# Performance work log

Hardware: AMD Instinct MI355X
Metric: run time of the kernel (lower is better)

Reference implementation:

```python
import jax, jax.numpy as jnp
import numpy as np

RATE = 0.5
N_NODES = 4096
N_EDGES = 131072
D_FEAT = 512


def setup_inputs() -> dict:
    key = jax.random.key(0)
    k1, k2, k3 = jax.random.split(key, 3)
    x = jax.random.normal(k1, (N_NODES, D_FEAT), dtype=jnp.float32)
    edge_index = jax.random.randint(k2, (2, N_EDGES), 0, N_NODES, dtype=jnp.int32)
    attention = jax.random.normal(k3, (N_EDGES, 1), dtype=jnp.float32)
    batch = jnp.zeros((N_NODES,), dtype=jnp.int32)
    return {"x": x, "edge_index": edge_index, "attention": attention,
            "batch": batch, "direction": 1}


def reference(x, edge_index, attention, batch, direction):
    N = x.shape[0]
    src = edge_index[0]
    dst = edge_index[1]

    # degree = torch.bincount(e_batch) over source nodes
    degree = jax.ops.segment_sum(jnp.ones_like(src, dtype=jnp.float32), src,
                                 num_segments=N)
    # g_pooling = segment mean of per-edge attention grouped by source node
    att_sum = jax.ops.segment_sum(attention[:, 0], src, num_segments=N)
    att_mean = jnp.where(degree > 0, att_sum / jnp.maximum(degree, 1.0), 0.0)
    # node_scores = direction * mean_attention * degree
    node_scores = direction * att_mean * degree

    # topk with ratio (single graph => k = ceil(rate * N)), sorted descending
    k = int(np.ceil(RATE * N))
    _, perm = jax.lax.top_k(node_scores, k)  # [k]

    # augment_adj: spspmm(A, A) -> 2-hop path counts; weights None -> ones
    A = jnp.zeros((N, N), dtype=jnp.float32).at[src, dst].add(1.0)
    A2 = A @ A  # [N, N] path counts; edges of augmented graph = nonzeros

    # filter_adj: keep edges among selected nodes, reindexed to [0, k)
    adj = (A2[perm][:, perm] > 0).astype(jnp.float32)  # [k, k] dense edge mask

    x_pooled = x[perm]            # [k, D]
    batch_pooled = batch[perm]    # [k]
    return (x_pooled, adj, batch_pooled, perm.reshape(1, -1))
```

## Files before the change

### kernel.cpp

```cpp
#include <hip/hip_runtime.h>

#define N_NODES 4096
#define N_EDGES 131072
#define D_FEAT  512
#define K_SEL   2048
#define MAXDEG  128
#define NWORDS  128

__global__ void zero_cnt(unsigned* __restrict__ cnt) {
    cnt[blockIdx.x * 256 + threadIdx.x] = 0u;
}

__global__ void build_kernel(const int* __restrict__ src, const int* __restrict__ dst,
                             unsigned* __restrict__ cnt, unsigned* __restrict__ slots) {
    int e = blockIdx.x * 512 + threadIdx.x;
    int s = src[e];
    int d = dst[e];
    unsigned pos = atomicAdd(&cnt[s], 1u);
    if (pos < MAXDEG) slots[((unsigned)s << 7) + pos] = ((unsigned)e << 12) | (unsigned)d;
}

__global__ void score_kernel(const unsigned* __restrict__ cnt,
                             const unsigned* __restrict__ slots,
                             const float* __restrict__ att,
                             const int* __restrict__ dir_p,
                             float* __restrict__ scores,
                             unsigned* __restrict__ B) {
    __shared__ float a_ord[4][MAXDEG];
    __shared__ unsigned brow[4][NWORDS];
    int t = threadIdx.x, wave = t >> 6, lane = t & 63;
    int n = blockIdx.x * 4 + wave;
    unsigned nb = (unsigned)n << 7;
    unsigned d = min(cnt[n], (unsigned)MAXDEG);
    unsigned v0 = (lane < (int)d)        ? slots[nb + lane]      : 0xFFFFFFFFu;
    unsigned v1 = ((lane + 64) < (int)d) ? slots[nb + lane + 64] : 0xFFFFFFFFu;

    brow[wave][lane] = 0u;
    brow[wave][lane + 64] = 0u;
    if (lane < (int)d)        atomicOr(&brow[wave][(v0 & 0xFFFu) >> 5], 1u << (v0 & 31));
    if ((lane + 64) < (int)d) atomicOr(&brow[wave][(v1 & 0xFFFu) >> 5], 1u << (v1 & 31));

    int r0 = 0, r1 = 0;
    int dk = (d < 64u) ? (int)d : 64;
    if (d <= 64u) {
        for (int k = 0; k < dk; ++k) {
            unsigned a = __shfl(v0, k);
            r0 += (a < v0);
        }
    } else {
        for (int k = 0; k < dk; ++k) {
            unsigned a = __shfl(v0, k);
            unsigned b = __shfl(v1, k);
            r0 += (a < v0) + (b < v0);
            r1 += (a < v1) + (b < v1);
        }
    }
    if (lane < (int)d)        a_ord[wave][r0] = att[v0 >> 12];
    if ((lane + 64) < (int)d) a_ord[wave][r1] = att[v1 >> 12];
    __syncthreads();

    B[nb + lane] = brow[wave][lane];
    B[nb + lane + 64] = brow[wave][lane + 64];

    if (lane == 0) {
        float sum = 0.0f;
        for (unsigned i = 0; i < d; ++i) sum += a_ord[wave][i];
        float score = 0.0f;
        if (d > 0) {
            float df = (float)d;
            float mean = sum / df;
            score = ((float)dir_p[0] * mean) * df;
        }
        scores[n] = score;
    }
}

__global__ void rank_kernel(const float* __restrict__ scores,
                            const int* __restrict__ batch,
                            const float* __restrict__ x,
                            unsigned* __restrict__ permw,
                            float* __restrict__ out_x,
                            float* __restrict__ out_batch,
                            float* __restrict__ out_perm) {
    int t = threadIdx.x, wave = t >> 6, lane = t & 63;
    int n = blockIdx.x * 4 + wave;
    float s = scores[n];
    const float4* sc4 = (const float4*)scores;
    int r = 0;
    #pragma unroll
    for (int i = 0; i < 16; ++i) {
        int q = lane + (i << 6);
        float4 v = sc4[q];
        int m = q << 2;
        r += (v.x > s) || (v.x == s && (m + 0) < n);
        r += (v.y > s) || (v.y == s && (m + 1) < n);
        r += (v.z > s) || (v.z == s && (m + 2) < n);
        r += (v.w > s) || (v.w == s && (m + 3) < n);
    }
    #pragma unroll
    for (int off = 32; off; off >>= 1) r += __shfl_down(r, off);
    r = __shfl(r, 0);
    if (r < K_SEL) {
        if (lane == 0) {
            permw[r] = (unsigned)n;
            out_perm[r] = (float)n;
            out_batch[r] = (float)batch[n];
        }
        const float4* xs = (const float4*)(x + (size_t)n * D_FEAT);
        float4* od = (float4*)(out_x + (size_t)r * D_FEAT);
        od[lane] = xs[lane];
        od[lane + 64] = xs[lane + 64];
    }
}

__global__ void adj_kernel(const unsigned* __restrict__ permw,
                           const unsigned* __restrict__ cnt,
                           const unsigned* __restrict__ slots,
                           const unsigned* __restrict__ B,
                           float* __restrict__ out_adj) {
    __shared__ unsigned nbr[MAXDEG];
    __shared__ unsigned rowH[2][NWORDS];
    int p = blockIdx.x, t = threadIdx.x;
    unsigned n = permw[p];
    unsigned d = min(cnt[n], (unsigned)MAXDEG);
    if (t < (int)d) nbr[t] = slots[((size_t)n << 7) + t] & 0xFFFu;
    __syncthreads();
    int w = t & 127, h = t >> 7;
    unsigned acc = 0;
    for (unsigned i = (unsigned)h; i < d; i += 2)
        acc |= B[((size_t)nbr[i] << 7) + w];
    rowH[h][w] = acc;
    __syncthreads();
    if (t < NWORDS) rowH[0][t] |= rowH[1][t];
    __syncthreads();
    float4* o4 = (float4*)(out_adj + (size_t)p * K_SEL);
    #pragma unroll
    for (int i = 0; i < 2; ++i) {
        int q4 = t + (i << 8);
        int q = q4 << 2;
        unsigned c0 = permw[q], c1 = permw[q + 1], c2 = permw[q + 2], c3 = permw[q + 3];
        float4 v;
        v.x = (float)((rowH[0][c0 >> 5] >> (c0 & 31)) & 1u);
        v.y = (float)((rowH[0][c1 >> 5] >> (c1 & 31)) & 1u);
        v.z = (float)((rowH[0][c2 >> 5] >> (c2 & 31)) & 1u);
        v.w = (float)((rowH[0][c3 >> 5] >> (c3 & 31)) & 1u);
        o4[q4] = v;
    }
}

extern "C" void kernel_launch(void* const* d_in, const int* in_sizes, int n_in,
                              void* d_out, int out_size, void* d_ws, size_t ws_size,
                              hipStream_t stream) {
    const float* x     = (const float*)d_in[0];
    const int*   eidx  = (const int*)d_in[1];
    const float* att   = (const float*)d_in[2];
    const int*   batch = (const int*)d_in[3];
    const int*   dir_p = (const int*)d_in[4];
    const int* src = eidx;
    const int* dst = eidx + N_EDGES;

    char* ws = (char*)d_ws;
    unsigned* B      = (unsigned*)(ws + 0);
    unsigned* cnt    = (unsigned*)(ws + 2097152);
    float*    scores = (float*)   (ws + 2113536);
    unsigned* permw  = (unsigned*)(ws + 2129920);
    unsigned* slots  = (unsigned*)(ws + 2138112);

    float* out_x     = (float*)d_out;
    float* out_adj   = out_x + (size_t)K_SEL * D_FEAT;
    float* out_batch = out_adj + (size_t)K_SEL * K_SEL;
    float* out_perm  = out_batch + K_SEL;

    zero_cnt<<<N_NODES / 256, 256, 0, stream>>>(cnt);
    build_kernel<<<N_EDGES / 512, 512, 0, stream>>>(src, dst, cnt, slots);
    score_kernel<<<N_NODES / 4, 256, 0, stream>>>(cnt, slots, att, dir_p, scores, B);
    rank_kernel<<<N_NODES / 4, 256, 0, stream>>>(scores, batch, x, permw,
                                                 out_x, out_batch, out_perm);
    adj_kernel<<<K_SEL, 256, 0, stream>>>(permw, cnt, slots, B, out_adj);
}
```

Baseline: 43.57 us.

## Fuse count, build and score into one node-owning kernel with shared-memory bucketing

Replaces the zero, global-atomic bucket build and score kernels with one kernel where each block owns 32 source nodes. The block scans the full src array and buckets matching edges into shared memory with shared atomics, then computes scores and bitmask rows. This removes two launches and the global atomics and slot round-trip, but every block now rereads the whole edge list and only 128 blocks are launched.

New measurement: 121.5 us. +178.8%, slower.

```diff
diff --git a/kernel.cpp b/kernel.cpp
--- a/kernel.cpp
+++ b/kernel.cpp
@@ -6,72 +6,97 @@
 #define K_SEL   2048
 #define MAXDEG  128
 #define NWORDS  128
-
-__global__ void zero_cnt(unsigned* __restrict__ cnt) {
-    cnt[blockIdx.x * 256 + threadIdx.x] = 0u;
-}
-
-__global__ void build_kernel(const int* __restrict__ src, const int* __restrict__ dst,
-                             unsigned* __restrict__ cnt, unsigned* __restrict__ slots) {
-    int e = blockIdx.x * 512 + threadIdx.x;
-    int s = src[e];
-    int d = dst[e];
-    unsigned pos = atomicAdd(&cnt[s], 1u);
-    if (pos < MAXDEG) slots[((unsigned)s << 7) + pos] = ((unsigned)e << 12) | (unsigned)d;
-}
-
-__global__ void score_kernel(const unsigned* __restrict__ cnt,
-                             const unsigned* __restrict__ slots,
-                             const float* __restrict__ att,
-                             const int* __restrict__ dir_p,
-                             float* __restrict__ scores,
-                             unsigned* __restrict__ B) {
-    __shared__ float a_ord[4][MAXDEG];
+#define OWN     32
+#define NBSS    (N_NODES / OWN)
+
+__global__ __launch_bounds__(256) void bss_kernel(
+    const int* __restrict__ src, const int* __restrict__ dst,
+    const float* __restrict__ att, const int* __restrict__ dir_p,
+    unsigned* __restrict__ cnt, unsigned* __restrict__ gslots,
+    unsigned* __restrict__ B, float* __restrict__ scores)
+{
+    __shared__ unsigned lcnt[OWN];
+    __shared__ unsigned lslots[OWN][MAXDEG];
+    __shared__ float    a_ord[4][MAXDEG];
     __shared__ unsigned brow[4][NWORDS];
-    int t = threadIdx.x, wave = t >> 6, lane = t & 63;
-    int n = blockIdx.x * 4 + wave;
-    unsigned nb = (unsigned)n << 7;
-    unsigned d = min(cnt[n], (unsigned)MAXDEG);
-    unsigned v0 = (lane < (int)d)        ? slots[nb + lane]      : 0xFFFFFFFFu;
-    unsigned v1 = ((lane + 64) < (int)d) ? slots[nb + lane + 64] : 0xFFFFFFFFu;
-
-    brow[wave][lane] = 0u;
-    brow[wave][lane + 64] = 0u;
-    if (lane < (int)d)        atomicOr(&brow[wave][(v0 & 0xFFFu) >> 5], 1u << (v0 & 31));
-    if ((lane + 64) < (int)d) atomicOr(&brow[wave][(v1 & 0xFFFu) >> 5], 1u << (v1 & 31));
-
-    int r0 = 0, r1 = 0;
-    int dk = (d < 64u) ? (int)d : 64;
-    if (d <= 64u) {
-        for (int k = 0; k < dk; ++k) {
-            unsigned a = __shfl(v0, k);
-            r0 += (a < v0);
+    const int t = threadIdx.x, wave = t >> 6, lane = t & 63;
+    const int base = blockIdx.x * OWN;
+
+    if (t < OWN) lcnt[t] = 0u;
+    __syncthreads();
+
+    const int4* s4 = (const int4*)src;
+    for (int i = t; i < N_EDGES / 4; i += 256) {
+        int4 v = s4[i];
+        int e0 = i << 2;
+        unsigned ls;
+        ls = (unsigned)(v.x - base);
+        if (ls < OWN) { unsigned p = atomicAdd(&lcnt[ls], 1u);
+            if (p < MAXDEG) lslots[ls][p] = ((unsigned)(e0 + 0) << 12) | (unsigned)dst[e0 + 0]; }
+        ls = (unsigned)(v.y - base);
+        if (ls < OWN) { unsigned p = atomicAdd(&lcnt[ls], 1u);
+            if (p < MAXDEG) lslots[ls][p] = ((unsigned)(e0 + 1) << 12) | (unsigned)dst[e0 + 1]; }
+        ls = (unsigned)(v.z - base);
+        if (ls < OWN) { unsigned p = atomicAdd(&lcnt[ls], 1u);
+            if (p < MAXDEG) lslots[ls][p] = ((unsigned)(e0 + 2) << 12) | (unsigned)dst[e0 + 2]; }
+        ls = (unsigned)(v.w - base);
+        if (ls < OWN) { unsigned p = atomicAdd(&lcnt[ls], 1u);
+            if (p < MAXDEG) lslots[ls][p] = ((unsigned)(e0 + 3) << 12) | (unsigned)dst[e0 + 3]; }
+    }
+    __syncthreads();
+
+    for (int it = 0; it < OWN / 4; ++it) {
+        __syncthreads();
+        int ln = (it << 2) + wave;
+        int n = base + ln;
+        unsigned d = min(lcnt[ln], (unsigned)MAXDEG);
+        unsigned v0 = (lane < (int)d)        ? lslots[ln][lane]      : 0xFFFFFFFFu;
+        unsigned v1 = ((lane + 64) < (int)d) ? lslots[ln][lane + 64] : 0xFFFFFFFFu;
+
+        float a0 = (lane < (int)d)        ? att[v0 >> 12] : 0.0f;
+        float a1 = ((lane + 64) < (int)d) ? att[v1 >> 12] : 0.0f;
+
+        brow[wave][lane] = 0u;
+        brow[wave][lane + 64] = 0u;
+        if (lane < (int)d)        atomicOr(&brow[wave][(v0 & 0xFFFu) >> 5], 1u << (v0 & 31));
+        if ((lane + 64) < (int)d) atomicOr(&brow[wave][(v1 & 0xFFFu) >> 5], 1u << (v1 & 31));
+
+        int r0 = 0, r1 = 0;
+        int dk = (d < 64u) ? (int)d : 64;
+        if (d <= 64u) {
+            for (int k = 0; k < dk; ++k) {
+                unsigned a = __shfl(v0, k);
+                r0 += (a < v0);
+            }
+        } else {
+            for (int k = 0; k < dk; ++k) {
+                unsigned a = __shfl(v0, k);
+                unsigned b = __shfl(v1, k);
+                r0 += (a < v0) + (b < v0);
+                r1 += (a < v1) + (b < v1);
+            }
         }
-    } else {
-        for (int k = 0; k < dk; ++k) {
-            unsigned a = __shfl(v0, k);
-            unsigned b = __shfl(v1, k);
-            r0 += (a < v0) + (b < v0);
-            r1 += (a < v1) + (b < v1);
+        if (lane < (int)d)        a_ord[wave][r0] = a0;
+        if ((lane + 64) < (int)d) a_ord[wave][r1] = a1;
+        __syncthreads();
+
+        if (lane == 0) {
+            float sum = 0.0f;
+            for (unsigned i = 0; i < d; ++i) sum += a_ord[wave][i];
+            float score = 0.0f;
+            if (d > 0) {
+                float df = (float)d;
+                float mean = sum / df;
+                score = ((float)dir_p[0] * mean) * df;
+            }
+            scores[n] = score;
+            cnt[n] = d;
         }
-    }
-    if (lane < (int)d)        a_ord[wave][r0] = att[v0 >> 12];
-    if ((lane + 64) < (int)d) a_ord[wave][r1] = att[v1 >> 12];
-    __syncthreads();
-
-    B[nb + lane] = brow[wave][lane];
-    B[nb + lane + 64] = brow[wave][lane + 64];
-
-    if (lane == 0) {
-        float sum = 0.0f;
-        for (unsigned i = 0; i < d; ++i) sum += a_ord[wave][i];
-        float score = 0.0f;
-        if (d > 0) {
-            float df = (float)d;
-            float mean = sum / df;
-            score = ((float)dir_p[0] * mean) * df;
-        }
-        scores[n] = score;
+        unsigned nb = (unsigned)n << 7;
+        B[nb + lane] = brow[wave][lane];
+        B[nb + lane + 64] = brow[wave][lane + 64];
+        if (lane < (int)d)        gslots[nb + lane] = v0;
+        if ((lane + 64) < (int)d) gslots[nb + lane + 64] = v1;
     }
 }
 
@@ -164,17 +189,15 @@
     unsigned* cnt    = (unsigned*)(ws + 2097152);
     float*    scores = (float*)   (ws + 2113536);
     unsigned* permw  = (unsigned*)(ws + 2129920);
-    unsigned* slots  = (unsigned*)(ws + 2138112);
+    unsigned* gslots = (unsigned*)(ws + 2138112);
 
     float* out_x     = (float*)d_out;
     float* out_adj   = out_x + (size_t)K_SEL * D_FEAT;
     float* out_batch = out_adj + (size_t)K_SEL * K_SEL;
     float* out_perm  = out_batch + K_SEL;
 
-    zero_cnt<<<N_NODES / 256, 256, 0, stream>>>(cnt);
-    build_kernel<<<N_EDGES / 512, 512, 0, stream>>>(src, dst, cnt, slots);
-    score_kernel<<<N_NODES / 4, 256, 0, stream>>>(cnt, slots, att, dir_p, scores, B);
+    bss_kernel<<<NBSS, 256, 0, stream>>>(src, dst, att, dir_p, cnt, gslots, B, scores);
     rank_kernel<<<N_NODES / 4, 256, 0, stream>>>(scores, batch, x, permw,
                                                  out_x, out_batch, out_perm);
-    adj_kernel<<<K_SEL, 256, 0, stream>>>(permw, cnt, slots, B, out_adj);
-}
+    adj_kernel<<<K_SEL, 256, 0, stream>>>(permw, cnt, gslots, B, out_adj);
+}
```

## Drop precomputed neighbor bitmask; build 2-hop rows from slots with LDS atomics

Applied to the files above, without the earlier changes.

Removes the per-node adjacency bitmask array B (2 MB) that score_kernel wrote and adj_kernel read. adj_kernel now gathers each neighbor's destination list directly from slots and sets bits in one shared row with LDS atomicOr, instead of OR-ing 128-word bitmask rows. The aim is to cut global write and read traffic for B. The cost is more scattered slot reads, an extra cnt lookup per neighbor, and LDS atomic contention. score_kernel also issues the attention gathers earlier and sums in float4 chunks.

Result: slower. 46.08 us (+5.8%).

```diff
diff --git a/kernel.cpp b/kernel.cpp
--- a/kernel.cpp
+++ b/kernel.cpp
@@ -24,10 +24,8 @@
                              const unsigned* __restrict__ slots,
                              const float* __restrict__ att,
                              const int* __restrict__ dir_p,
-                             float* __restrict__ scores,
-                             unsigned* __restrict__ B) {
+                             float* __restrict__ scores) {
     __shared__ float a_ord[4][MAXDEG];
-    __shared__ unsigned brow[4][NWORDS];
     int t = threadIdx.x, wave = t >> 6, lane = t & 63;
     int n = blockIdx.x * 4 + wave;
     unsigned nb = (unsigned)n << 7;
@@ -35,10 +33,8 @@
     unsigned v0 = (lane < (int)d)        ? slots[nb + lane]      : 0xFFFFFFFFu;
     unsigned v1 = ((lane + 64) < (int)d) ? slots[nb + lane + 64] : 0xFFFFFFFFu;
 
-    brow[wave][lane] = 0u;
-    brow[wave][lane + 64] = 0u;
-    if (lane < (int)d)        atomicOr(&brow[wave][(v0 & 0xFFFu) >> 5], 1u << (v0 & 31));
-    if ((lane + 64) < (int)d) atomicOr(&brow[wave][(v1 & 0xFFFu) >> 5], 1u << (v1 & 31));
+    float a0 = (lane < (int)d)        ? att[v0 >> 12] : 0.0f;
+    float a1 = ((lane + 64) < (int)d) ? att[v1 >> 12] : 0.0f;
 
     int r0 = 0, r1 = 0;
     int dk = (d < 64u) ? (int)d : 64;
@@ -55,16 +51,18 @@
             r1 += (a < v1) + (b < v1);
         }
     }
-    if (lane < (int)d)        a_ord[wave][r0] = att[v0 >> 12];
-    if ((lane + 64) < (int)d) a_ord[wave][r1] = att[v1 >> 12];
+    if (lane < (int)d)        a_ord[wave][r0] = a0;
+    if ((lane + 64) < (int)d) a_ord[wave][r1] = a1;
     __syncthreads();
-
-    B[nb + lane] = brow[wave][lane];
-    B[nb + lane + 64] = brow[wave][lane + 64];
 
     if (lane == 0) {
         float sum = 0.0f;
-        for (unsigned i = 0; i < d; ++i) sum += a_ord[wave][i];
+        unsigned i = 0;
+        for (; i + 4 <= d; i += 4) {
+            float4 q = *(const float4*)&a_ord[wave][i];
+            sum += q.x; sum += q.y; sum += q.z; sum += q.w;
+        }
+        for (; i < d; ++i) sum += a_ord[wave][i];
         float score = 0.0f;
         if (d > 0) {
             float df = (float)d;
@@ -116,22 +114,27 @@
 __global__ void adj_kernel(const unsigned* __restrict__ permw,
                            const unsigned* __restrict__ cnt,
                            const unsigned* __restrict__ slots,
-                           const unsigned* __restrict__ B,
                            float* __restrict__ out_adj) {
     __shared__ unsigned nbr[MAXDEG];
-    __shared__ unsigned rowH[2][NWORDS];
+    __shared__ unsigned dnb[MAXDEG];
+    __shared__ unsigned row[NWORDS];
     int p = blockIdx.x, t = threadIdx.x;
     unsigned n = permw[p];
     unsigned d = min(cnt[n], (unsigned)MAXDEG);
-    if (t < (int)d) nbr[t] = slots[((size_t)n << 7) + t] & 0xFFFu;
+    if (t < NWORDS) row[t] = 0u;
+    if (t < (int)d) {
+        unsigned m = slots[((size_t)n << 7) + t] & 0xFFFu;
+        nbr[t] = m;
+        dnb[t] = min(cnt[m], (unsigned)MAXDEG);
+    }
     __syncthreads();
     int w = t & 127, h = t >> 7;
-    unsigned acc = 0;
-    for (unsigned i = (unsigned)h; i < d; i += 2)
-        acc |= B[((size_t)nbr[i] << 7) + w];
-    rowH[h][w] = acc;
-    __syncthreads();
-    if (t < NWORDS) rowH[0][t] |= rowH[1][t];
+    for (unsigned i = (unsigned)h; i < d; i += 2) {
+        if (w < (int)dnb[i]) {
+            unsigned dv = slots[((size_t)nbr[i] << 7) + w] & 0xFFFu;
+            atomicOr(&row[dv >> 5], 1u << (dv & 31));
+        }
+    }
     __syncthreads();
     float4* o4 = (float4*)(out_adj + (size_t)p * K_SEL);
     #pragma unroll
@@ -140,10 +143,10 @@
         int q = q4 << 2;
         unsigned c0 = permw[q], c1 = permw[q + 1], c2 = permw[q + 2], c3 = permw[q + 3];
         float4 v;
-        v.x = (float)((rowH[0][c0 >> 5] >> (c0 & 31)) & 1u);
-        v.y = (float)((rowH[0][c1 >> 5] >> (c1 & 31)) & 1u);
-        v.z = (float)((rowH[0][c2 >> 5] >> (c2 & 31)) & 1u);
-        v.w = (float)((rowH[0][c3 >> 5] >> (c3 & 31)) & 1u);
+        v.x = (float)((row[c0 >> 5] >> (c0 & 31)) & 1u);
+        v.y = (float)((row[c1 >> 5] >> (c1 & 31)) & 1u);
+        v.z = (float)((row[c2 >> 5] >> (c2 & 31)) & 1u);
+        v.w = (float)((row[c3 >> 5] >> (c3 & 31)) & 1u);
         o4[q4] = v;
     }
 }
@@ -160,11 +163,10 @@
     const int* dst = eidx + N_EDGES;
 
     char* ws = (char*)d_ws;
-    unsigned* B      = (unsigned*)(ws + 0);
-    unsigned* cnt    = (unsigned*)(ws + 2097152);
-    float*    scores = (float*)   (ws + 2113536);
-    unsigned* permw  = (unsigned*)(ws + 2129920);
-    unsigned* slots  = (unsigned*)(ws + 2138112);
+    unsigned* cnt    = (unsigned*)(ws + 0);
+    float*    scores = (float*)   (ws + 16384);
+    unsigned* permw  = (unsigned*)(ws + 32768);
+    unsigned* slots  = (unsigned*)(ws + 40960);
 
     float* out_x     = (float*)d_out;
     float* out_adj   = out_x + (size_t)K_SEL * D_FEAT;
@@ -173,8 +175,8 @@
 
     zero_cnt<<<N_NODES / 256, 256, 0, stream>>>(cnt);
     build_kernel<<<N_EDGES / 512, 512, 0, stream>>>(src, dst, cnt, slots);
-    score_kernel<<<N_NODES / 4, 256, 0, stream>>>(cnt, slots, att, dir_p, scores, B);
+    score_kernel<<<N_NODES / 4, 256, 0, stream>>>(cnt, slots, att, dir_p, scores);
     rank_kernel<<<N_NODES / 4, 256, 0, stream>>>(scores, batch, x, permw,
                                                  out_x, out_batch, out_perm);
-    adj_kernel<<<K_SEL, 256, 0, stream>>>(permw, cnt, slots, B, out_adj);
+    adj_kernel<<<K_SEL, 256, 0, stream>>>(permw, cnt, slots, out_adj);
 }
```
